# Kernel tuning notes

Hardware: AMD Instinct MI355X
Metric: run time of the kernel (lower is better)

## Reference

```python
import jax, jax.numpy as jnp
import numpy as np

NUM_GROUPS = 32
EPS = 1e-05
HT_MIN = -1.0
HT_MAX = 1.0


def setup_inputs() -> dict:
    key = jax.random.key(0)
    k1, k2, k3 = jax.random.split(key, 3)
    B, IN, OUT = 4096, 2048, 2048
    x = jax.random.normal(k1, (B, IN), dtype=jnp.float32)
    # kaiming-uniform-ish scale for weight, uniform bias bound 1/sqrt(in)
    weight = jax.random.normal(k2, (OUT, IN), dtype=jnp.float32) * (1.0 / np.sqrt(IN))
    bias = jax.random.uniform(k3, (OUT,), dtype=jnp.float32, minval=-1.0 / np.sqrt(IN), maxval=1.0 / np.sqrt(IN))
    gn_weight = jnp.ones((OUT,), dtype=jnp.float32)
    gn_bias = jnp.zeros((OUT,), dtype=jnp.float32)
    return {"x": x, "weight": weight, "bias": bias, "gn_weight": gn_weight, "gn_bias": gn_bias}


def reference(x, weight, bias, gn_weight, gn_bias):
    # Linear: y = x @ W^T + b   -> [B, OUT]
    y = jnp.einsum("bi,oi->bo", x, weight) + bias
    B, C = y.shape
    G = NUM_GROUPS
    yg = y.reshape(B, G, C // G)
    mean = jnp.mean(yg, axis=-1, keepdims=True)
    var = jnp.mean(jnp.square(yg), axis=-1, keepdims=True) - jnp.square(mean)
    yn = ((yg - mean) * jax.lax.rsqrt(var + EPS)).reshape(B, C)
    out = yn * gn_weight + gn_bias
    return jnp.clip(out, HT_MIN, HT_MAX)
```

## Files before the change

kernel.cpp:

```cpp
#include <hip/hip_runtime.h>
#include <stdint.h>

#define B_ROWS 4096
#define C_OUT  2048
#define C_IN   2048
#define EPS    1e-5f

typedef __attribute__((ext_vector_type(8))) short bf16x8;
typedef __attribute__((ext_vector_type(4))) float f32x4;

__device__ __forceinline__ unsigned short f2bf(float f) {
    uint32_t u = __float_as_uint(f);
    uint32_t r = (u + 0x7fffu + ((u >> 16) & 1u)) >> 16;
    return (unsigned short)r;
}

__global__ void cvt_f32_bf16_kernel(const float* __restrict__ x,
                                    const float* __restrict__ w,
                                    unsigned short* __restrict__ xb,
                                    unsigned short* __restrict__ wb,
                                    int nx4, int nw4) {
    int i = blockIdx.x * blockDim.x + threadIdx.x;
    const float* src;
    unsigned short* dst;
    if (i < nx4) {
        src = x; dst = xb;
    } else {
        i -= nx4;
        if (i >= nw4) return;
        src = w; dst = wb;
    }
    float4 v = ((const float4*)src)[i];
    ushort4 o;
    o.x = f2bf(v.x); o.y = f2bf(v.y); o.z = f2bf(v.z); o.w = f2bf(v.w);
    ((ushort4*)dst)[i] = o;
}

__global__ __launch_bounds__(128, 2)
void gemm_gn_kernel(const unsigned short* __restrict__ A,
                    const unsigned short* __restrict__ W,
                    const float* __restrict__ bias,
                    const float* __restrict__ gnw,
                    const float* __restrict__ gnb,
                    float* __restrict__ out) {
    __shared__ __align__(16) unsigned short sA[128 * 64];
    __shared__ __align__(16) unsigned short sB[64 * 64];

    const int bc   = blockIdx.x;
    const int br   = blockIdx.y;
    const int t    = threadIdx.x;
    const int lane = t & 63;
    const int wave = t >> 6;
    const int c16  = lane & 15;
    const int quad = lane >> 4;

    f32x4 acc[4][4];
#pragma unroll
    for (int i = 0; i < 4; i++)
#pragma unroll
        for (int j = 0; j < 4; j++) acc[i][j] = (f32x4){0.f, 0.f, 0.f, 0.f};

    const int r0 = t >> 3;
    const int qo = ((t & 7) ^ (r0 & 7)) * 8;
    const unsigned short* gA = A + (size_t)(br * 128 + r0) * C_IN + qo;
    const unsigned short* gB = W + (size_t)(bc * 64 + r0) * C_IN + qo;

    const int cl7 = c16 & 7;

    for (int k0 = 0; k0 < C_IN; k0 += 64) {
#pragma unroll
        for (int n = 0; n < 8; n++)
            __builtin_amdgcn_global_load_lds(
                (const __attribute__((address_space(1))) void*)(gA + (size_t)(n * 16) * C_IN + k0),
                (__attribute__((address_space(3))) void*)(sA + n * 1024 + t * 8), 16, 0, 0);
#pragma unroll
        for (int n = 0; n < 4; n++)
            __builtin_amdgcn_global_load_lds(
                (const __attribute__((address_space(1))) void*)(gB + (size_t)(n * 16) * C_IN + k0),
                (__attribute__((address_space(3))) void*)(sB + n * 1024 + t * 8), 16, 0, 0);
        __syncthreads();

#pragma unroll
        for (int sub = 0; sub < 2; sub++) {
            const int qs = ((sub << 2) | quad) ^ cl7;
            bf16x8 a[4], b[4];
#pragma unroll
            for (int i = 0; i < 4; i++)
                a[i] = *(const bf16x8*)(sA + (wave * 64 + i * 16 + c16) * 64 + qs * 8);
#pragma unroll
            for (int j = 0; j < 4; j++)
                b[j] = *(const bf16x8*)(sB + (j * 16 + c16) * 64 + qs * 8);
#pragma unroll
            for (int i = 0; i < 4; i++)
#pragma unroll
                for (int j = 0; j < 4; j++)
                    acc[i][j] = __builtin_amdgcn_mfma_f32_16x16x32_bf16(a[i], b[j], acc[i][j], 0, 0, 0);
        }
        __syncthreads();
    }

    const int colbase = bc * 64;
    const int rowbase = br * 128 + wave * 64;
    float bv[4], gw[4], gb[4];
#pragma unroll
    for (int j = 0; j < 4; j++) {
        int col = colbase + j * 16 + c16;
        bv[j] = bias[col];
        gw[j] = gnw[col];
        gb[j] = gnb[col];
    }
#pragma unroll
    for (int i = 0; i < 4; i++) {
#pragma unroll
        for (int r = 0; r < 4; r++) {
            float s = 0.f, ss = 0.f;
#pragma unroll
            for (int j = 0; j < 4; j++) {
                float v = acc[i][j][r] + bv[j];
                acc[i][j][r] = v;
                s += v;
                ss += v * v;
            }
#pragma unroll
            for (int m = 1; m < 16; m <<= 1) {
                s  += __shfl_xor(s, m, 64);
                ss += __shfl_xor(ss, m, 64);
            }
            float mean = s * (1.f / 64.f);
            float var  = ss * (1.f / 64.f) - mean * mean;
            float rstd = rsqrtf(var + EPS);
            int row = rowbase + i * 16 + quad * 4 + r;
            float* orow = out + (size_t)row * C_OUT;
#pragma unroll
            for (int j = 0; j < 4; j++) {
                float v = (acc[i][j][r] - mean) * rstd * gw[j] + gb[j];
                v = fminf(1.f, fmaxf(-1.f, v));
                orow[colbase + j * 16 + c16] = v;
            }
        }
    }
}

extern "C" void kernel_launch(void* const* d_in, const int* in_sizes, int n_in,
                              void* d_out, int out_size, void* d_ws, size_t ws_size,
                              hipStream_t stream) {
    const float* x    = (const float*)d_in[0];
    const float* w    = (const float*)d_in[1];
    const float* bias = (const float*)d_in[2];
    const float* gnw  = (const float*)d_in[3];
    const float* gnb  = (const float*)d_in[4];
    float* out = (float*)d_out;

    unsigned short* xb = (unsigned short*)d_ws;
    unsigned short* wb = xb + (size_t)B_ROWS * C_IN;

    const int nx4 = B_ROWS * C_IN / 4;
    const int nw4 = C_OUT * C_IN / 4;
    cvt_f32_bf16_kernel<<<(nx4 + nw4 + 255) / 256, 256, 0, stream>>>(x, w, xb, wb, nx4, nw4);

    dim3 grid(C_OUT / 64, B_ROWS / 128);
    gemm_gn_kernel<<<grid, 128, 0, stream>>>(xb, wb, bias, gnw, gnb, out);
}
```

Measured before the change: 147.0 us.

## Split K across wave pairs with LDS reduction of partial accumulators

Doubles the block to 256 threads so each pair of waves handles one half of every 64-wide K slice (intra-k split), and the two halves are summed through LDS before the GroupNorm epilogue. The goal is more waves per CU for latency hiding and fewer LDS reads per wave per iteration. In exchange it adds a two-phase LDS reduction with extra barriers at the end, and half the waves sit idle during the epilogue.

```diff
diff --git a/kernel.cpp b/kernel.cpp
--- a/kernel.cpp
+++ b/kernel.cpp
@@ -36,7 +36,7 @@
     ((ushort4*)dst)[i] = o;
 }
 
-__global__ __launch_bounds__(128, 2)
+__global__ __launch_bounds__(256, 3)
 void gemm_gn_kernel(const unsigned short* __restrict__ A,
                     const unsigned short* __restrict__ W,
                     const float* __restrict__ bias,
@@ -51,6 +51,8 @@
     const int t    = threadIdx.x;
     const int lane = t & 63;
     const int wave = t >> 6;
+    const int wr   = wave & 1;
+    const int kh   = wave >> 1;
     const int c16  = lane & 15;
     const int quad = lane >> 4;
 
@@ -65,42 +67,67 @@
     const unsigned short* gA = A + (size_t)(br * 128 + r0) * C_IN + qo;
     const unsigned short* gB = W + (size_t)(bc * 64 + r0) * C_IN + qo;
 
-    const int cl7 = c16 & 7;
+    const int qs = (((kh << 2) | quad) ^ (c16 & 7)) * 8;
 
     for (int k0 = 0; k0 < C_IN; k0 += 64) {
 #pragma unroll
-        for (int n = 0; n < 8; n++)
-            __builtin_amdgcn_global_load_lds(
-                (const __attribute__((address_space(1))) void*)(gA + (size_t)(n * 16) * C_IN + k0),
-                (__attribute__((address_space(3))) void*)(sA + n * 1024 + t * 8), 16, 0, 0);
-#pragma unroll
         for (int n = 0; n < 4; n++)
             __builtin_amdgcn_global_load_lds(
-                (const __attribute__((address_space(1))) void*)(gB + (size_t)(n * 16) * C_IN + k0),
-                (__attribute__((address_space(3))) void*)(sB + n * 1024 + t * 8), 16, 0, 0);
+                (const __attribute__((address_space(1))) void*)(gA + (size_t)(n * 32) * C_IN + k0),
+                (__attribute__((address_space(3))) void*)(sA + n * 2048 + t * 8), 16, 0, 0);
+#pragma unroll
+        for (int n = 0; n < 2; n++)
+            __builtin_amdgcn_global_load_lds(
+                (const __attribute__((address_space(1))) void*)(gB + (size_t)(n * 32) * C_IN + k0),
+                (__attribute__((address_space(3))) void*)(sB + n * 2048 + t * 8), 16, 0, 0);
         __syncthreads();
 
+        bf16x8 a[4], b[4];
 #pragma unroll
-        for (int sub = 0; sub < 2; sub++) {
-            const int qs = ((sub << 2) | quad) ^ cl7;
-            bf16x8 a[4], b[4];
+        for (int i = 0; i < 4; i++)
+            a[i] = *(const bf16x8*)(sA + (wr * 64 + i * 16 + c16) * 64 + qs);
 #pragma unroll
-            for (int i = 0; i < 4; i++)
-                a[i] = *(const bf16x8*)(sA + (wave * 64 + i * 16 + c16) * 64 + qs * 8);
+        for (int j = 0; j < 4; j++)
+            b[j] = *(const bf16x8*)(sB + (j * 16 + c16) * 64 + qs);
+#pragma unroll
+        for (int i = 0; i < 4; i++)
 #pragma unroll
             for (int j = 0; j < 4; j++)
-                b[j] = *(const bf16x8*)(sB + (j * 16 + c16) * 64 + qs * 8);
+                acc[i][j] = __builtin_amdgcn_mfma_f32_16x16x32_bf16(a[i], b[j], acc[i][j], 0, 0, 0);
+        __syncthreads();
+    }
+
+    float* fbuf = (float*)sA;
 #pragma unroll
-            for (int i = 0; i < 4; i++)
+    for (int ph = 0; ph < 2; ph++) {
+        if (kh == 1) {
+#pragma unroll
+            for (int ii = 0; ii < 2; ii++) {
+                int i = ph * 2 + ii;
 #pragma unroll
                 for (int j = 0; j < 4; j++)
-                    acc[i][j] = __builtin_amdgcn_mfma_f32_16x16x32_bf16(a[i], b[j], acc[i][j], 0, 0, 0);
+                    *(f32x4*)(fbuf + wr * 2048 + ii * 1024 + (j * 16 + c16) * 16 + quad * 4) = acc[i][j];
+            }
+        }
+        __syncthreads();
+        if (kh == 0) {
+#pragma unroll
+            for (int ii = 0; ii < 2; ii++) {
+                int i = ph * 2 + ii;
+#pragma unroll
+                for (int j = 0; j < 4; j++) {
+                    f32x4 v = *(const f32x4*)(fbuf + wr * 2048 + ii * 1024 + (j * 16 + c16) * 16 + quad * 4);
+                    acc[i][j] += v;
+                }
+            }
         }
         __syncthreads();
     }
 
+    if (kh == 1) return;
+
     const int colbase = bc * 64;
-    const int rowbase = br * 128 + wave * 64;
+    const int rowbase = br * 128 + wr * 64;
     float bv[4], gw[4], gb[4];
 #pragma unroll
     for (int j = 0; j < 4; j++) {
@@ -159,5 +186,5 @@
     cvt_f32_bf16_kernel<<<(nx4 + nw4 + 255) / 256, 256, 0, stream>>>(x, w, xb, wb, nx4, nw4);
 
     dim3 grid(C_OUT / 64, B_ROWS / 128);
-    gemm_gn_kernel<<<grid, 128, 0, stream>>>(xb, wb, bias, gnw, gnb, out);
+    gemm_gn_kernel<<<grid, 256, 0, stream>>>(xb, wb, bias, gnw, gnb, out);
 }
```

Result: no change. 148.3 us (+0.9%).

## Double-buffer LDS tiles, split K across wave pairs, and swizzle block order

Applied to the files above, without the earlier changes.

Moves the GEMM to 256 threads per block, where two wave pairs each handle one half of every 64-wide K tile and their partial accumulators are reduced through LDS before the GroupNorm epilogue. Loads into LDS are double-buffered so the next K tile's global_load_lds is issued before the current tile is consumed, leaving one barrier per iteration. Blocks are launched on a 1D grid remapped so that 16 consecutive blocks share an A row-block, which is meant to improve L2 reuse. The cost is twice the shared memory, an extra LDS reduction, and half the waves sitting idle during the epilogue.

```diff
diff --git a/kernel.cpp b/kernel.cpp
--- a/kernel.cpp
+++ b/kernel.cpp
@@ -36,21 +36,23 @@
     ((ushort4*)dst)[i] = o;
 }
 
-__global__ __launch_bounds__(128, 2)
+__global__ __launch_bounds__(256, 3)
 void gemm_gn_kernel(const unsigned short* __restrict__ A,
                     const unsigned short* __restrict__ W,
                     const float* __restrict__ bias,
                     const float* __restrict__ gnw,
                     const float* __restrict__ gnb,
                     float* __restrict__ out) {
-    __shared__ __align__(16) unsigned short sA[128 * 64];
-    __shared__ __align__(16) unsigned short sB[64 * 64];
+    __shared__ __align__(16) unsigned short smem[2 * 12288];
 
-    const int bc   = blockIdx.x;
-    const int br   = blockIdx.y;
+    const int flat = blockIdx.x;
+    const int br   = (flat >> 4) & 31;
+    const int bc   = (flat & 15) | ((flat >> 9) << 4);
     const int t    = threadIdx.x;
     const int lane = t & 63;
     const int wave = t >> 6;
+    const int wr   = wave & 1;
+    const int kh   = wave >> 1;
     const int c16  = lane & 15;
     const int quad = lane >> 4;
 
@@ -65,42 +67,66 @@
     const unsigned short* gA = A + (size_t)(br * 128 + r0) * C_IN + qo;
     const unsigned short* gB = W + (size_t)(bc * 64 + r0) * C_IN + qo;
 
-    const int cl7 = c16 & 7;
+    const int qs = (((kh << 2) | quad) ^ (c16 & 7)) * 8;
 
-    for (int k0 = 0; k0 < C_IN; k0 += 64) {
+#define STAGE(buf, k0)                                                                     \
+    do {                                                                                   \
+        unsigned short* sa = smem + (buf) * 12288;                                         \
+        unsigned short* sb = sa + 8192;                                                    \
+        _Pragma("unroll")                                                                  \
+        for (int n = 0; n < 4; n++)                                                        \
+            __builtin_amdgcn_global_load_lds(                                              \
+                (const __attribute__((address_space(1))) void*)(gA + (size_t)(n * 32) * C_IN + (k0)), \
+                (__attribute__((address_space(3))) void*)(sa + n * 2048 + t * 8), 16, 0, 0); \
+        _Pragma("unroll")                                                                  \
+        for (int n = 0; n < 2; n++)                                                        \
+            __builtin_amdgcn_global_load_lds(                                              \
+                (const __attribute__((address_space(1))) void*)(gB + (size_t)(n * 32) * C_IN + (k0)), \
+                (__attribute__((address_space(3))) void*)(sb + n * 2048 + t * 8), 16, 0, 0); \
+    } while (0)
+
+    STAGE(0, 0);
+    int cur = 0;
+    for (int it = 0; it < 32; ++it) {
+        __syncthreads();
+        if (it < 31) STAGE(cur ^ 1, (it + 1) * 64);
+
+        const unsigned short* sa = smem + cur * 12288;
+        const unsigned short* sb = sa + 8192;
+        bf16x8 a[4], b[4];
 #pragma unroll
-        for (int n = 0; n < 8; n++)
-            __builtin_amdgcn_global_load_lds(
-                (const __attribute__((address_space(1))) void*)(gA + (size_t)(n * 16) * C_IN + k0),
-                (__attribute__((address_space(3))) void*)(sA + n * 1024 + t * 8), 16, 0, 0);
+        for (int i = 0; i < 4; i++)
+            a[i] = *(const bf16x8*)(sa + (wr * 64 + i * 16 + c16) * 64 + qs);
 #pragma unroll
-        for (int n = 0; n < 4; n++)
-            __builtin_amdgcn_global_load_lds(
-                (const __attribute__((address_space(1))) void*)(gB + (size_t)(n * 16) * C_IN + k0),
-                (__attribute__((address_space(3))) void*)(sB + n * 1024 + t * 8), 16, 0, 0);
-        __syncthreads();
-
+        for (int j = 0; j < 4; j++)
+            b[j] = *(const bf16x8*)(sb + (j * 16 + c16) * 64 + qs);
 #pragma unroll
-        for (int sub = 0; sub < 2; sub++) {
-            const int qs = ((sub << 2) | quad) ^ cl7;
-            bf16x8 a[4], b[4];
-#pragma unroll
-            for (int i = 0; i < 4; i++)
-                a[i] = *(const bf16x8*)(sA + (wave * 64 + i * 16 + c16) * 64 + qs * 8);
+        for (int i = 0; i < 4; i++)
 #pragma unroll
             for (int j = 0; j < 4; j++)
-                b[j] = *(const bf16x8*)(sB + (j * 16 + c16) * 64 + qs * 8);
-#pragma unroll
-            for (int i = 0; i < 4; i++)
-#pragma unroll
-                for (int j = 0; j < 4; j++)
-                    acc[i][j] = __builtin_amdgcn_mfma_f32_16x16x32_bf16(a[i], b[j], acc[i][j], 0, 0, 0);
-        }
-        __syncthreads();
+                acc[i][j] = __builtin_amdgcn_mfma_f32_16x16x32_bf16(a[i], b[j], acc[i][j], 0, 0, 0);
+        cur ^= 1;
     }
 
+    __syncthreads();
+    float* fbuf = (float*)smem;
+    if (kh == 1) {
+#pragma unroll
+        for (int i = 0; i < 4; i++)
+#pragma unroll
+            for (int j = 0; j < 4; j++)
+                *(f32x4*)(fbuf + wr * 4096 + i * 1024 + j * 256 + lane * 4) = acc[i][j];
+    }
+    __syncthreads();
+    if (kh == 1) return;
+#pragma unroll
+    for (int i = 0; i < 4; i++)
+#pragma unroll
+        for (int j = 0; j < 4; j++)
+            acc[i][j] += *(const f32x4*)(fbuf + wr * 4096 + i * 1024 + j * 256 + lane * 4);
+
     const int colbase = bc * 64;
-    const int rowbase = br * 128 + wave * 64;
+    const int rowbase = br * 128 + wr * 64;
     float bv[4], gw[4], gb[4];
 #pragma unroll
     for (int j = 0; j < 4; j++) {
@@ -158,6 +184,5 @@
     const int nw4 = C_OUT * C_IN / 4;
     cvt_f32_bf16_kernel<<<(nx4 + nw4 + 255) / 256, 256, 0, stream>>>(x, w, xb, wb, nx4, nw4);
 
-    dim3 grid(C_OUT / 64, B_ROWS / 128);
-    gemm_gn_kernel<<<grid, 128, 0, stream>>>(xb, wb, bias, gnw, gnb, out);
+    gemm_gn_kernel<<<1024, 256, 0, stream>>>(xb, wb, bias, gnw, gnb, out);
 }
```

Measured after the change: 151.4 us. 1.03x slower.
